# Kernel optimization log

Measured on AMD Instinct MI355X. Metric: run time of the kernel, lower is better.

## Reference

```python
import jax, jax.numpy as jnp
import numpy as np

N_HEAD = 16
D_HEAD = 64
SCALE = 1.0 / D_HEAD ** 0.5


def setup_inputs() -> dict:
    key = jax.random.key(0)
    k1, k2, k3, k4 = jax.random.split(key, 4)
    bsz, qlen, d_embed, d_model = 4, 1024, 768, 1024
    return {
        "word_emb": jax.random.normal(k1, (bsz, qlen, d_embed), dtype=jnp.float32),
        "emb_w": jax.random.normal(k2, (d_embed, d_model), dtype=jnp.float32) * 0.02,
        "emb_b": jnp.zeros((d_model,), dtype=jnp.float32),
        "qkv_w0": jax.random.normal(k3, (d_model, 3 * N_HEAD * D_HEAD), dtype=jnp.float32) * 0.02,
        "qkv_w1": jax.random.normal(k4, (d_model, 3 * N_HEAD * D_HEAD), dtype=jnp.float32) * 0.02,
    }


def _mha(h, qkv_w):
    # h: [qlen, bsz, d_model]
    qlen, bsz, _ = h.shape
    heads = h @ qkv_w  # [qlen, bsz, 3*n_head*d_head]
    head_q, head_k, head_v = jnp.split(heads, 3, axis=-1)
    head_q = head_q.reshape(qlen, bsz, N_HEAD, D_HEAD)
    head_k = head_k.reshape(qlen, bsz, N_HEAD, D_HEAD)
    head_v = head_v.reshape(qlen, bsz, N_HEAD, D_HEAD)
    # explicit score materialization, faithful to the source einsum pattern
    attn_score = jnp.einsum('ibnd,jbnd->ijbn', head_q, head_k) * SCALE
    attn_prob = jax.nn.softmax(attn_score, axis=1)  # softmax over klen (dim=1)
    attn_vec = jnp.einsum('ijbn,jbnd->ibnd', attn_prob, head_v)
    attn_vec = attn_vec.reshape(qlen, bsz, N_HEAD * D_HEAD)
    return attn_vec, attn_prob


def reference(word_emb, emb_w, emb_b, qkv_w0, qkv_w1):
    # word_emb: [bsz, qlen, d_embed] -> [qlen, bsz, d_embed]
    h = jnp.transpose(word_emb, (1, 0, 2))
    h = h @ emb_w + emb_b  # emb_proj since d_embed != d_model
    # NOTE: the source computes pos_emb and word_emb + pos_emb, but then
    # overwrites with core_out = self.drop(word_emb), discarding pos_emb.
    # Dropout is identity in reference (eval) mode, so core_out == h.
    core_out = h
    core_out, attn_maps = _mha(core_out, qkv_w0)
    core_out, attn_maps = _mha(core_out, qkv_w1)
    return core_out, attn_maps
```

## Files before the change

### kernel.cpp

```cpp
#include <hip/hip_runtime.h>

#define LOG2E 1.44269504088896340736f

typedef __attribute__((ext_vector_type(8))) short short8;
typedef __attribute__((ext_vector_type(4))) short short4v;
typedef __attribute__((ext_vector_type(4))) float floatx4;

__device__ __forceinline__ float bf2f(short s) {
    union { float f; unsigned u; } v; v.u = ((unsigned)(unsigned short)s) << 16; return v.f;
}
__device__ __forceinline__ short f2bf(float f) {
    union { float f; unsigned u; } v; v.f = f;
    unsigned u = v.u;
    u += 0x7FFFu + ((u >> 16) & 1u);
    return (short)(u >> 16);
}

__device__ __forceinline__ void gl_lds16(const void* g, void* l) {
    __builtin_amdgcn_global_load_lds((const __attribute__((address_space(1))) void*)g,
                                     (__attribute__((address_space(3))) void*)l, 16, 0, 0);
}

__device__ __forceinline__ void wcast_tile(const float* __restrict__ W,
                                           short* __restrict__ Wt, int K, int N,
                                           int n0, int k0, int t) {
    __shared__ float tile[64][65];
    int r = t >> 2, c4 = (t & 3) * 16;
    const float* src = W + (size_t)(k0 + r) * N + n0 + c4;
#pragma unroll
    for (int q = 0; q < 16; ++q) tile[r][c4 + q] = src[q];
    __syncthreads();
    short* dst = Wt + (size_t)(n0 + r) * K + k0 + c4;
    short8 o1, o2;
#pragma unroll
    for (int q = 0; q < 8; ++q) o1[q] = f2bf(tile[c4 + q][r]);
#pragma unroll
    for (int q = 0; q < 8; ++q) o2[q] = f2bf(tile[c4 + 8 + q][r]);
    *(short8*)(dst) = o1;
    *(short8*)(dst + 8) = o2;
}

__global__ __launch_bounds__(256) void prep(const float* __restrict__ we,
                                            const float* __restrict__ emb_w,
                                            const float* __restrict__ qkv_w0,
                                            const float* __restrict__ qkv_w1,
                                            short* __restrict__ A0,
                                            short* __restrict__ WtE,
                                            short* __restrict__ Wt0,
                                            short* __restrict__ Wt1) {
    int bid = blockIdx.x, t = threadIdx.x;
    if (bid < 1536) {
        int e = bid * 256 + t;
        int m = e / 96, dc = (e % 96) * 8;
        int b = m & 3, s = m >> 2;
        const float* src = we + (size_t)(b * 1024 + s) * 768 + dc;
        short8 o;
#pragma unroll
        for (int q = 0; q < 8; ++q) o[q] = f2bf(src[q]);
        *(short8*)(A0 + (size_t)m * 768 + dc) = o;
    } else if (bid < 1728) {
        int tt = bid - 1536;
        wcast_tile(emb_w, WtE, 768, 1024, (tt & 15) * 64, (tt >> 4) * 64, t);
    } else if (bid < 2496) {
        int tt = bid - 1728;
        wcast_tile(qkv_w0, Wt0, 1024, 3072, (tt % 48) * 64, (tt / 48) * 64, t);
    } else {
        int tt = bid - 2496;
        wcast_tile(qkv_w1, Wt1, 1024, 3072, (tt % 48) * 64, (tt / 48) * 64, t);
    }
}

template <int PACK>
__global__ __launch_bounds__(256) void gemm_bt(const short* __restrict__ A,
                                               const short* __restrict__ Bt,
                                               short* __restrict__ C,
                                               const float* __restrict__ bias,
                                               int K, int N,
                                               short* __restrict__ Qp,
                                               short* __restrict__ Kp,
                                               short* __restrict__ Vp) {
    __shared__ __align__(16) short sA[128 * 64];
    __shared__ __align__(16) short sB[128 * 64];
    int n0 = blockIdx.x * 128, m0 = blockIdx.y * 128;
    int tid = threadIdx.x;
    int lane = tid & 63, w = tid >> 6;
    int wm = (w >> 1) * 64, wn = (w & 1) * 64;
    int l15 = lane & 15, quad = lane >> 4;
    int lrow = lane >> 3, lchunk = (lane & 7) ^ lrow;

    floatx4 zero = {0.f, 0.f, 0.f, 0.f};
    floatx4 acc[4][4];
#pragma unroll
    for (int i = 0; i < 4; ++i)
#pragma unroll
        for (int j = 0; j < 4; ++j) acc[i][j] = zero;

    for (int k0 = 0; k0 < K; k0 += 64) {
#pragma unroll
        for (int c = 0; c < 4; ++c) {
            int r0 = w * 32 + c * 8;
            int row = r0 + lrow;
            gl_lds16(A + (size_t)(m0 + row) * K + k0 + lchunk * 8, sA + r0 * 64);
            gl_lds16(Bt + (size_t)(n0 + row) * K + k0 + lchunk * 8, sB + r0 * 64);
        }
        __syncthreads();
#pragma unroll
        for (int h = 0; h < 2; ++h) {
            int sw = ((h * 4 + quad) ^ (l15 & 7)) * 8;
            short8 af[4], bfr[4];
#pragma unroll
            for (int i = 0; i < 4; ++i) {
                af[i]  = *(const short8*)(sA + (wm + i * 16 + l15) * 64 + sw);
                bfr[i] = *(const short8*)(sB + (wn + i * 16 + l15) * 64 + sw);
            }
#pragma unroll
            for (int i = 0; i < 4; ++i)
#pragma unroll
                for (int j = 0; j < 4; ++j)
                    acc[i][j] = __builtin_amdgcn_mfma_f32_16x16x32_bf16(bfr[j], af[i], acc[i][j], 0, 0, 0);
        }
        __syncthreads();
    }
#pragma unroll
    for (int i = 0; i < 4; ++i) {
        int row = m0 + wm + i * 16 + l15;
#pragma unroll
        for (int j = 0; j < 4; ++j) {
            int colb = n0 + wn + j * 16 + quad * 4;
            if (PACK == 0) {
                float4 bv = bias ? *(const float4*)(bias + colb) : float4{0.f, 0.f, 0.f, 0.f};
                short4v st;
                st[0] = f2bf(acc[i][j][0] + bv.x);
                st[1] = f2bf(acc[i][j][1] + bv.y);
                st[2] = f2bf(acc[i][j][2] + bv.z);
                st[3] = f2bf(acc[i][j][3] + bv.w);
                *(short4v*)(C + (size_t)row * N + colb) = st;
            } else {
                int sel = colb >> 10, nn = colb & 1023;
                int bn = ((row & 3) << 4) + (nn >> 6);
                size_t idx = (size_t)bn * 65536 + (size_t)(row >> 2) * 64 + (nn & 63);
                float sc = (sel == 0) ? 0.125f : 1.0f;
                short4v st;
#pragma unroll
                for (int r = 0; r < 4; ++r) st[r] = f2bf(acc[i][j][r] * sc);
                short* dst = (sel == 0) ? Qp : (sel == 1 ? Kp : Vp);
                *(short4v*)(dst + idx) = st;
            }
        }
    }
}

__global__ __launch_bounds__(256) void pack_v(const short* __restrict__ Vp,
                                              short* __restrict__ Vtp) {
    __shared__ short vt[64][72];
    int bn = blockIdx.y;
    int t0 = blockIdx.x * 64;
    int t = threadIdx.x;
#pragma unroll
    for (int h = 0; h < 2; ++h) {
        int c = t + h * 256;
        int tt = c >> 3, off = (c & 7) * 8;
        short8 v = *(const short8*)(Vp + (size_t)bn * 65536 + (size_t)(t0 + tt) * 64 + off);
#pragma unroll
        for (int e = 0; e < 8; ++e) vt[tt][off + e] = v[e];
    }
    __syncthreads();
#pragma unroll
    for (int h = 0; h < 2; ++h) {
        int c = t + h * 256;
        int d = c >> 3, joff = (c & 7) * 8;
        short8 o;
#pragma unroll
        for (int e = 0; e < 8; ++e) o[e] = vt[joff + e][d];
        *(short8*)(Vtp + (size_t)bn * 65536 + (size_t)d * 1024 + t0 + joff) = o;
    }
}

template <bool L2>
__global__ __launch_bounds__(64) void fattn(const short* __restrict__ Qp,
                                            const short* __restrict__ Kp,
                                            const short* __restrict__ Vtp,
                                            void* __restrict__ Optr,
                                            float* __restrict__ linv,
                                            short* __restrict__ Pp) {
    __shared__ __align__(16) short plds[32 * 32];
    int bid = blockIdx.x;
    int xcd = bid & 7, wid = bid >> 3;
    int bn = xcd * 8 + (wid >> 5);
    int i0 = (wid & 31) * 32;
    int b = bn >> 4, n = bn & 15;
    int lane = threadIdx.x, l15 = lane & 15, quad = lane >> 4;
    const short* Qb = Qp + (size_t)bn * 65536;
    const short* Kb = Kp + (size_t)bn * 65536;
    const short* Vb = Vtp + (size_t)bn * 65536;

    short8 qf[2][2];
#pragma unroll
    for (int ib = 0; ib < 2; ++ib) {
        qf[ib][0] = *(const short8*)(Qb + (i0 + ib * 16 + l15) * 64 + quad * 8);
        qf[ib][1] = *(const short8*)(Qb + (i0 + ib * 16 + l15) * 64 + 32 + quad * 8);
    }
    floatx4 zero = {0.f, 0.f, 0.f, 0.f};
    floatx4 o[2][4];
#pragma unroll
    for (int ib = 0; ib < 2; ++ib)
#pragma unroll
        for (int tt = 0; tt < 4; ++tt) o[ib][tt] = zero;
    float lsum[2] = {0.f, 0.f};

    for (int j0 = 0; j0 < 1024; j0 += 32) {
#pragma unroll
        for (int jb = 0; jb < 2; ++jb) {
            const short* kr = Kb + (j0 + jb * 16 + l15) * 64 + quad * 8;
            short8 kf0 = *(const short8*)(kr);
            short8 kf1 = *(const short8*)(kr + 32);
#pragma unroll
            for (int ib = 0; ib < 2; ++ib) {
                floatx4 s = zero;
                s = __builtin_amdgcn_mfma_f32_16x16x32_bf16(kf0, qf[ib][0], s, 0, 0, 0);
                s = __builtin_amdgcn_mfma_f32_16x16x32_bf16(kf1, qf[ib][1], s, 0, 0, 0);
                short4v pk;
                float ls = 0.f;
#pragma unroll
                for (int r = 0; r < 4; ++r) {
                    float p = __builtin_amdgcn_exp2f(s[r] * LOG2E);
                    ls += p;
                    pk[r] = f2bf(p);
                }
                lsum[ib] += ls;
                *(short4v*)(plds + (ib * 16 + l15) * 32 + jb * 16 + quad * 4) = pk;
                if (L2) {
                    *(short4v*)(Pp + (size_t)bn * 1048576 +
                                (size_t)(i0 + ib * 16 + l15) * 1024 + j0 + jb * 16 + quad * 4) = pk;
                }
            }
        }
        __syncthreads();
        short8 pa[2];
        pa[0] = *(const short8*)(plds + l15 * 32 + quad * 8);
        pa[1] = *(const short8*)(plds + (16 + l15) * 32 + quad * 8);
#pragma unroll
        for (int tt = 0; tt < 4; ++tt) {
            short8 vf = *(const short8*)(Vb + (tt * 16 + l15) * 1024 + j0 + quad * 8);
#pragma unroll
            for (int ib = 0; ib < 2; ++ib)
                o[ib][tt] = __builtin_amdgcn_mfma_f32_16x16x32_bf16(vf, pa[ib], o[ib][tt], 0, 0, 0);
        }
        __syncthreads();
    }
    float rinv[2];
#pragma unroll
    for (int ib = 0; ib < 2; ++ib) {
        float t = lsum[ib];
        t += __shfl_xor(t, 16);
        t += __shfl_xor(t, 32);
        rinv[ib] = 1.f / t;
    }
    if (L2 && quad == 0) {
        linv[bn * 1024 + i0 + l15] = rinv[0];
        linv[bn * 1024 + i0 + 16 + l15] = rinv[1];
    }
#pragma unroll
    for (int ib = 0; ib < 2; ++ib)
#pragma unroll
        for (int tt = 0; tt < 4; ++tt) {
            int row = i0 + ib * 16 + l15;
            int colb = n * 64 + tt * 16 + quad * 4;
            size_t idx = (size_t)(row * 4 + b) * 1024 + colb;
            if (L2) {
                float4 v;
                v.x = o[ib][tt][0] * rinv[ib];
                v.y = o[ib][tt][1] * rinv[ib];
                v.z = o[ib][tt][2] * rinv[ib];
                v.w = o[ib][tt][3] * rinv[ib];
                *(float4*)((float*)Optr + idx) = v;
            } else {
                short4v st;
#pragma unroll
                for (int r = 0; r < 4; ++r) st[r] = f2bf(o[ib][tt][r] * rinv[ib]);
                *(short4v*)((short*)Optr + idx) = st;
            }
        }
}

__global__ __launch_bounds__(256) void pfin(const short* __restrict__ Pp,
                                            const float* __restrict__ linv,
                                            float* __restrict__ Pout) {
    __shared__ short sP[64 * 512];
    int j0 = blockIdx.x * 32, i0 = blockIdx.y * 16;
    int t = threadIdx.x;
#pragma unroll
    for (int h = 0; h < 16; ++h) {
        int c = t + h * 256;
        int bn = c >> 6, rem = c & 63, ii = rem >> 2, part = rem & 3;
        short8 v = *(const short8*)(Pp + (size_t)bn * 1048576 +
                                    (size_t)(i0 + ii) * 1024 + j0 + part * 8);
        float li = linv[bn * 1024 + i0 + ii];
        short8 sv;
#pragma unroll
        for (int e = 0; e < 8; ++e) sv[e] = f2bf(bf2f(v[e]) * li);
        *(short8*)(sP + bn * 512 + ii * 32 + part * 8) = sv;
    }
    __syncthreads();
    int ii = t >> 4, q = t & 15;
    float* dst = Pout + (size_t)(i0 + ii) * 65536 + j0 * 64 + q * 128;
#pragma unroll
    for (int e4 = 0; e4 < 32; ++e4) {
        int pos = q * 128 + e4 * 4;
        int jj = pos >> 6, bnb = pos & 63;
        float4 v;
        v.x = bf2f(sP[(bnb + 0) * 512 + ii * 32 + jj]);
        v.y = bf2f(sP[(bnb + 1) * 512 + ii * 32 + jj]);
        v.z = bf2f(sP[(bnb + 2) * 512 + ii * 32 + jj]);
        v.w = bf2f(sP[(bnb + 3) * 512 + ii * 32 + jj]);
        *(float4*)(dst + e4 * 4) = v;
    }
}

extern "C" void kernel_launch(void* const* d_in, const int* in_sizes, int n_in,
                              void* d_out, int out_size, void* d_ws, size_t ws_size,
                              hipStream_t stream) {
    const float* word_emb = (const float*)d_in[0];
    const float* emb_w    = (const float*)d_in[1];
    const float* emb_b    = (const float*)d_in[2];
    const float* qkv_w0   = (const float*)d_in[3];
    const float* qkv_w1   = (const float*)d_in[4];
    float* out0 = (float*)d_out;
    float* out1 = out0 + 4194304;

    char* ws = (char*)d_ws;
    short* A0    = (short*)(ws);
    short* WtE   = (short*)(ws + 6291456);
    short* Wt0   = (short*)(ws + 7864320);
    short* Wt1   = (short*)(ws + 14155776);
    short* hbuf  = (short*)(ws + 20447232);
    short* h2    = (short*)(ws + 28835840);
    short* Qp    = (short*)(ws + 37224448);
    short* Kp    = (short*)(ws + 45613056);
    short* Vp    = (short*)(ws + 54001664);
    short* Vtp   = (short*)(ws + 62390272);
    float* linv  = (float*)(ws + 70778880);
    short* Pp    = (short*)(ws + 71041024);

    prep<<<3264, 256, 0, stream>>>(word_emb, emb_w, qkv_w0, qkv_w1, A0, WtE, Wt0, Wt1);

    gemm_bt<0><<<dim3(8, 32), 256, 0, stream>>>(A0, WtE, hbuf, emb_b, 768, 1024,
                                                nullptr, nullptr, nullptr);
    gemm_bt<1><<<dim3(24, 32), 256, 0, stream>>>(hbuf, Wt0, nullptr, nullptr, 1024, 3072,
                                                 Qp, Kp, Vp);
    pack_v<<<dim3(16, 64), 256, 0, stream>>>(Vp, Vtp);
    fattn<false><<<2048, 64, 0, stream>>>(Qp, Kp, Vtp, (void*)h2, nullptr, nullptr);
    gemm_bt<1><<<dim3(24, 32), 256, 0, stream>>>(h2, Wt1, nullptr, nullptr, 1024, 3072,
                                                 Qp, Kp, Vp);
    pack_v<<<dim3(16, 64), 256, 0, stream>>>(Vp, Vtp);
    fattn<true><<<2048, 64, 0, stream>>>(Qp, Kp, Vtp, (void*)out0, linv, Pp);
    pfin<<<dim3(32, 64), 256, 0, stream>>>(Pp, linv, out1);
}
```

Baseline: 683.3 us.

## Prefetch K/V into registers and double-buffer P in attention; vectorize prep loads

The attention kernel now loads the next 32-key block of K and V into registers while it computes scores and PV products for the current block. The P tile in LDS is double-buffered, and both per-iteration __syncthreads are removed; since a block is a single 64-lane wavefront, LDS ordering within the wave is relied on instead. The aim is to hide global-load latency behind MFMA and exp work. In exchange, register usage goes up, which may lower occupancy. Separately, the prep cast kernels switch from scalar float loads to float4 loads.

New measurement: 688.7 us. About the same (+0.8%).

```diff
diff --git a/kernel.cpp b/kernel.cpp
--- a/kernel.cpp
+++ b/kernel.cpp
@@ -27,8 +27,14 @@
     __shared__ float tile[64][65];
     int r = t >> 2, c4 = (t & 3) * 16;
     const float* src = W + (size_t)(k0 + r) * N + n0 + c4;
-#pragma unroll
-    for (int q = 0; q < 16; ++q) tile[r][c4 + q] = src[q];
+    float4 f0 = *(const float4*)(src);
+    float4 f1 = *(const float4*)(src + 4);
+    float4 f2 = *(const float4*)(src + 8);
+    float4 f3 = *(const float4*)(src + 12);
+    tile[r][c4 + 0] = f0.x;  tile[r][c4 + 1] = f0.y;  tile[r][c4 + 2] = f0.z;  tile[r][c4 + 3] = f0.w;
+    tile[r][c4 + 4] = f1.x;  tile[r][c4 + 5] = f1.y;  tile[r][c4 + 6] = f1.z;  tile[r][c4 + 7] = f1.w;
+    tile[r][c4 + 8] = f2.x;  tile[r][c4 + 9] = f2.y;  tile[r][c4 + 10] = f2.z; tile[r][c4 + 11] = f2.w;
+    tile[r][c4 + 12] = f3.x; tile[r][c4 + 13] = f3.y; tile[r][c4 + 14] = f3.z; tile[r][c4 + 15] = f3.w;
     __syncthreads();
     short* dst = Wt + (size_t)(n0 + r) * K + k0 + c4;
     short8 o1, o2;
@@ -54,9 +60,11 @@
         int m = e / 96, dc = (e % 96) * 8;
         int b = m & 3, s = m >> 2;
         const float* src = we + (size_t)(b * 1024 + s) * 768 + dc;
+        float4 f0 = *(const float4*)(src);
+        float4 f1 = *(const float4*)(src + 4);
         short8 o;
-#pragma unroll
-        for (int q = 0; q < 8; ++q) o[q] = f2bf(src[q]);
+        o[0] = f2bf(f0.x); o[1] = f2bf(f0.y); o[2] = f2bf(f0.z); o[3] = f2bf(f0.w);
+        o[4] = f2bf(f1.x); o[5] = f2bf(f1.y); o[6] = f2bf(f1.z); o[7] = f2bf(f1.w);
         *(short8*)(A0 + (size_t)m * 768 + dc) = o;
     } else if (bid < 1728) {
         int tt = bid - 1536;
@@ -183,7 +191,7 @@
                                             void* __restrict__ Optr,
                                             float* __restrict__ linv,
                                             short* __restrict__ Pp) {
-    __shared__ __align__(16) short plds[32 * 32];
+    __shared__ __align__(16) short plds[2][32 * 32];
     int bid = blockIdx.x;
     int xcd = bid & 7, wid = bid >> 3;
     int bn = xcd * 8 + (wid >> 5);
@@ -208,17 +216,38 @@
         for (int tt = 0; tt < 4; ++tt) o[ib][tt] = zero;
     float lsum[2] = {0.f, 0.f};
 
+    short8 kc[2][2], vc[4], kn[2][2], vn[4];
+#pragma unroll
+    for (int jb = 0; jb < 2; ++jb) {
+        const short* kr = Kb + (jb * 16 + l15) * 64 + quad * 8;
+        kc[jb][0] = *(const short8*)(kr);
+        kc[jb][1] = *(const short8*)(kr + 32);
+    }
+#pragma unroll
+    for (int tt = 0; tt < 4; ++tt)
+        vc[tt] = *(const short8*)(Vb + (tt * 16 + l15) * 1024 + quad * 8);
+
+    int buf = 0;
+#pragma unroll 2
     for (int j0 = 0; j0 < 1024; j0 += 32) {
+        if (j0 + 32 < 1024) {
+#pragma unroll
+            for (int jb = 0; jb < 2; ++jb) {
+                const short* kr = Kb + (j0 + 32 + jb * 16 + l15) * 64 + quad * 8;
+                kn[jb][0] = *(const short8*)(kr);
+                kn[jb][1] = *(const short8*)(kr + 32);
+            }
+#pragma unroll
+            for (int tt = 0; tt < 4; ++tt)
+                vn[tt] = *(const short8*)(Vb + (tt * 16 + l15) * 1024 + j0 + 32 + quad * 8);
+        }
 #pragma unroll
         for (int jb = 0; jb < 2; ++jb) {
-            const short* kr = Kb + (j0 + jb * 16 + l15) * 64 + quad * 8;
-            short8 kf0 = *(const short8*)(kr);
-            short8 kf1 = *(const short8*)(kr + 32);
 #pragma unroll
             for (int ib = 0; ib < 2; ++ib) {
                 floatx4 s = zero;
-                s = __builtin_amdgcn_mfma_f32_16x16x32_bf16(kf0, qf[ib][0], s, 0, 0, 0);
-                s = __builtin_amdgcn_mfma_f32_16x16x32_bf16(kf1, qf[ib][1], s, 0, 0, 0);
+                s = __builtin_amdgcn_mfma_f32_16x16x32_bf16(kc[jb][0], qf[ib][0], s, 0, 0, 0);
+                s = __builtin_amdgcn_mfma_f32_16x16x32_bf16(kc[jb][1], qf[ib][1], s, 0, 0, 0);
                 short4v pk;
                 float ls = 0.f;
 #pragma unroll
@@ -228,25 +257,26 @@
                     pk[r] = f2bf(p);
                 }
                 lsum[ib] += ls;
-                *(short4v*)(plds + (ib * 16 + l15) * 32 + jb * 16 + quad * 4) = pk;
+                *(short4v*)(plds[buf] + (ib * 16 + l15) * 32 + jb * 16 + quad * 4) = pk;
                 if (L2) {
                     *(short4v*)(Pp + (size_t)bn * 1048576 +
                                 (size_t)(i0 + ib * 16 + l15) * 1024 + j0 + jb * 16 + quad * 4) = pk;
                 }
             }
         }
-        __syncthreads();
         short8 pa[2];
-        pa[0] = *(const short8*)(plds + l15 * 32 + quad * 8);
-        pa[1] = *(const short8*)(plds + (16 + l15) * 32 + quad * 8);
-#pragma unroll
-        for (int tt = 0; tt < 4; ++tt) {
-            short8 vf = *(const short8*)(Vb + (tt * 16 + l15) * 1024 + j0 + quad * 8);
+        pa[0] = *(const short8*)(plds[buf] + l15 * 32 + quad * 8);
+        pa[1] = *(const short8*)(plds[buf] + (16 + l15) * 32 + quad * 8);
+#pragma unroll
+        for (int tt = 0; tt < 4; ++tt)
 #pragma unroll
             for (int ib = 0; ib < 2; ++ib)
-                o[ib][tt] = __builtin_amdgcn_mfma_f32_16x16x32_bf16(vf, pa[ib], o[ib][tt], 0, 0, 0);
-        }
-        __syncthreads();
+                o[ib][tt] = __builtin_amdgcn_mfma_f32_16x16x32_bf16(vc[tt], pa[ib], o[ib][tt], 0, 0, 0);
+#pragma unroll
+        for (int jb = 0; jb < 2; ++jb) { kc[jb][0] = kn[jb][0]; kc[jb][1] = kn[jb][1]; }
+#pragma unroll
+        for (int tt = 0; tt < 4; ++tt) vc[tt] = vn[tt];
+        buf ^= 1;
     }
     float rinv[2];
 #pragma unroll
```

## Share K/V tiles across four waves via double-buffered LDS in attention

Applied to the files above, without the earlier changes.

The attention kernel now runs four 64-lane waves per block, each handling 32 query rows of a 128-row block. K and transposed-V tiles are staged into LDS with async global-to-LDS loads, using XOR swizzling for K, padding for V and double buffering so the next tile is fetched during compute. This replaces per-wave direct global reads, cutting redundant K/V traffic by sharing each tile among four waves. The prep kernel also switches its fp32 loads to float4 vector loads; the block barrier per iteration now couples four waves and raises LDS use per block.

Result: faster. 628.0 us (-8.1%).

```diff
diff --git a/kernel.cpp b/kernel.cpp
--- a/kernel.cpp
+++ b/kernel.cpp
@@ -27,8 +27,14 @@
     __shared__ float tile[64][65];
     int r = t >> 2, c4 = (t & 3) * 16;
     const float* src = W + (size_t)(k0 + r) * N + n0 + c4;
-#pragma unroll
-    for (int q = 0; q < 16; ++q) tile[r][c4 + q] = src[q];
+    float4 f0 = *(const float4*)(src);
+    float4 f1 = *(const float4*)(src + 4);
+    float4 f2 = *(const float4*)(src + 8);
+    float4 f3 = *(const float4*)(src + 12);
+    tile[r][c4 + 0] = f0.x;  tile[r][c4 + 1] = f0.y;  tile[r][c4 + 2] = f0.z;  tile[r][c4 + 3] = f0.w;
+    tile[r][c4 + 4] = f1.x;  tile[r][c4 + 5] = f1.y;  tile[r][c4 + 6] = f1.z;  tile[r][c4 + 7] = f1.w;
+    tile[r][c4 + 8] = f2.x;  tile[r][c4 + 9] = f2.y;  tile[r][c4 + 10] = f2.z; tile[r][c4 + 11] = f2.w;
+    tile[r][c4 + 12] = f3.x; tile[r][c4 + 13] = f3.y; tile[r][c4 + 14] = f3.z; tile[r][c4 + 15] = f3.w;
     __syncthreads();
     short* dst = Wt + (size_t)(n0 + r) * K + k0 + c4;
     short8 o1, o2;
@@ -54,9 +60,11 @@
         int m = e / 96, dc = (e % 96) * 8;
         int b = m & 3, s = m >> 2;
         const float* src = we + (size_t)(b * 1024 + s) * 768 + dc;
+        float4 f0 = *(const float4*)(src);
+        float4 f1 = *(const float4*)(src + 4);
         short8 o;
-#pragma unroll
-        for (int q = 0; q < 8; ++q) o[q] = f2bf(src[q]);
+        o[0] = f2bf(f0.x); o[1] = f2bf(f0.y); o[2] = f2bf(f0.z); o[3] = f2bf(f0.w);
+        o[4] = f2bf(f1.x); o[5] = f2bf(f1.y); o[6] = f2bf(f1.z); o[7] = f2bf(f1.w);
         *(short8*)(A0 + (size_t)m * 768 + dc) = o;
     } else if (bid < 1728) {
         int tt = bid - 1536;
@@ -177,22 +185,47 @@
 }
 
 template <bool L2>
-__global__ __launch_bounds__(64) void fattn(const short* __restrict__ Qp,
-                                            const short* __restrict__ Kp,
-                                            const short* __restrict__ Vtp,
-                                            void* __restrict__ Optr,
-                                            float* __restrict__ linv,
-                                            short* __restrict__ Pp) {
-    __shared__ __align__(16) short plds[32 * 32];
+__global__ __launch_bounds__(256) void fattn(const short* __restrict__ Qp,
+                                             const short* __restrict__ Kp,
+                                             const short* __restrict__ Vtp,
+                                             void* __restrict__ Optr,
+                                             float* __restrict__ linv,
+                                             short* __restrict__ Pp) {
+    __shared__ __align__(16) short sK[2][32 * 64];
+    __shared__ __align__(16) short sV[2][64 * 40];
+    __shared__ __align__(16) short plds[4][2][32 * 32];
     int bid = blockIdx.x;
-    int xcd = bid & 7, wid = bid >> 3;
-    int bn = xcd * 8 + (wid >> 5);
-    int i0 = (wid & 31) * 32;
+    int xcd = bid & 7, rr = bid >> 3;
+    int bn = xcd * 8 + (rr & 7);
+    int iblk = rr >> 3;
+    int tid = threadIdx.x, w = tid >> 6, lane = tid & 63;
+    int i0 = iblk * 128 + w * 32;
     int b = bn >> 4, n = bn & 15;
-    int lane = threadIdx.x, l15 = lane & 15, quad = lane >> 4;
+    int l15 = lane & 15, quad = lane >> 4;
     const short* Qb = Qp + (size_t)bn * 65536;
-    const short* Kb = Kp + (size_t)bn * 65536;
-    const short* Vb = Vtp + (size_t)bn * 65536;
+    const char* Kb = (const char*)(Kp + (size_t)bn * 65536);
+    const char* Vb = (const char*)(Vtp + (size_t)bn * 65536);
+
+    int kr_ = lane >> 3, ko_ = lane & 7;
+    size_t koff = (size_t)kr_ * 128 + ((ko_ ^ kr_) * 16);
+    int vr_[5], vc_[5];
+#pragma unroll
+    for (int c = 0; c < 5; ++c) {
+        int beta = c * 1024 + lane * 16;
+        vr_[c] = beta / 80;
+        vc_[c] = (beta % 80) & 63;
+    }
+
+#define KCALL(B, J0, c) \
+    gl_lds16(Kb + (size_t)((J0) + 8 * (c)) * 128 + koff, (char*)sK[B] + (c) * 1024)
+#define VCALL(B, J0, c) \
+    gl_lds16(Vb + (size_t)vr_[c] * 2048 + (size_t)(J0) * 2 + vc_[c], (char*)sV[B] + (c) * 1024)
+#define STAGE(B, J0) do { \
+        if (w == 0)      { KCALL(B, J0, 0); KCALL(B, J0, 1); } \
+        else if (w == 1) { KCALL(B, J0, 2); KCALL(B, J0, 3); } \
+        else if (w == 2) { VCALL(B, J0, 0); VCALL(B, J0, 1); VCALL(B, J0, 2); } \
+        else             { VCALL(B, J0, 3); VCALL(B, J0, 4); } \
+    } while (0)
 
     short8 qf[2][2];
 #pragma unroll
@@ -208,12 +241,20 @@
         for (int tt = 0; tt < 4; ++tt) o[ib][tt] = zero;
     float lsum[2] = {0.f, 0.f};
 
+    STAGE(0, 0);
+    __syncthreads();
+
+    int buf = 0;
+#pragma unroll 2
     for (int j0 = 0; j0 < 1024; j0 += 32) {
+        if (j0 + 32 < 1024) STAGE(buf ^ 1, j0 + 32);
+        short* pw = plds[w][buf];
+        int r7 = l15 & 7;
 #pragma unroll
         for (int jb = 0; jb < 2; ++jb) {
-            const short* kr = Kb + (j0 + jb * 16 + l15) * 64 + quad * 8;
-            short8 kf0 = *(const short8*)(kr);
-            short8 kf1 = *(const short8*)(kr + 32);
+            const short* kbase = sK[buf] + (jb * 16 + l15) * 64;
+            short8 kf0 = *(const short8*)(kbase + ((quad ^ r7) * 8));
+            short8 kf1 = *(const short8*)(kbase + (((4 + quad) ^ r7) * 8));
 #pragma unroll
             for (int ib = 0; ib < 2; ++ib) {
                 floatx4 s = zero;
@@ -228,26 +269,30 @@
                     pk[r] = f2bf(p);
                 }
                 lsum[ib] += ls;
-                *(short4v*)(plds + (ib * 16 + l15) * 32 + jb * 16 + quad * 4) = pk;
+                *(short4v*)(pw + (ib * 16 + l15) * 32 + jb * 16 + quad * 4) = pk;
                 if (L2) {
                     *(short4v*)(Pp + (size_t)bn * 1048576 +
                                 (size_t)(i0 + ib * 16 + l15) * 1024 + j0 + jb * 16 + quad * 4) = pk;
                 }
             }
         }
-        __syncthreads();
         short8 pa[2];
-        pa[0] = *(const short8*)(plds + l15 * 32 + quad * 8);
-        pa[1] = *(const short8*)(plds + (16 + l15) * 32 + quad * 8);
+        pa[0] = *(const short8*)(pw + l15 * 32 + quad * 8);
+        pa[1] = *(const short8*)(pw + (16 + l15) * 32 + quad * 8);
 #pragma unroll
         for (int tt = 0; tt < 4; ++tt) {
-            short8 vf = *(const short8*)(Vb + (tt * 16 + l15) * 1024 + j0 + quad * 8);
+            short8 vf = *(const short8*)(sV[buf] + (tt * 16 + l15) * 40 + quad * 8);
 #pragma unroll
             for (int ib = 0; ib < 2; ++ib)
                 o[ib][tt] = __builtin_amdgcn_mfma_f32_16x16x32_bf16(vf, pa[ib], o[ib][tt], 0, 0, 0);
         }
         __syncthreads();
-    }
+        buf ^= 1;
+    }
+#undef STAGE
+#undef KCALL
+#undef VCALL
+
     float rinv[2];
 #pragma unroll
     for (int ib = 0; ib < 2; ++ib) {
@@ -349,10 +394,10 @@
     gemm_bt<1><<<dim3(24, 32), 256, 0, stream>>>(hbuf, Wt0, nullptr, nullptr, 1024, 3072,
                                                  Qp, Kp, Vp);
     pack_v<<<dim3(16, 64), 256, 0, stream>>>(Vp, Vtp);
-    fattn<false><<<2048, 64, 0, stream>>>(Qp, Kp, Vtp, (void*)h2, nullptr, nullptr);
+    fattn<false><<<512, 256, 0, stream>>>(Qp, Kp, Vtp, (void*)h2, nullptr, nullptr);
     gemm_bt<1><<<dim3(24, 32), 256, 0, stream>>>(h2, Wt1, nullptr, nullptr, 1024, 3072,
                                                  Qp, Kp, Vp);
     pack_v<<<dim3(16, 64), 256, 0, stream>>>(Vp, Vtp);
-    fattn<true><<<2048, 64, 0, stream>>>(Qp, Kp, Vtp, (void*)out0, linv, Pp);
+    fattn<true><<<512, 256, 0, stream>>>(Qp, Kp, Vtp, (void*)out0, linv, Pp);
     pfin<<<dim3(32, 64), 256, 0, stream>>>(Pp, linv, out1);
 }
```
